# Optimization experiments

Measured on AMD Instinct MI355X. Metric: run time of the kernel, lower is better.

Reference implementation:

```python
import jax, jax.numpy as jnp
import numpy as np

BATCH, T, N_STATE, N_IN, N_OUT = 256, 4096, 32, 8, 8
DT = 1e-3


def setup_inputs() -> dict:
    key = jax.random.key(0)
    k_u, k_x0, k_A, k_B, k_C, k_D = jax.random.split(key, 6)
    t = jnp.arange(T, dtype=jnp.float32) * DT
    u = jax.random.normal(k_u, (BATCH, T, N_IN), dtype=jnp.float32)
    x0 = jax.random.normal(k_x0, (BATCH, N_STATE), dtype=jnp.float32)
    # Stable-ish LTI system parameters
    A = (0.1 / np.sqrt(N_STATE)) * jax.random.normal(k_A, (N_STATE, N_STATE), dtype=jnp.float32) - 0.5 * jnp.eye(N_STATE, dtype=jnp.float32)
    B = jax.random.normal(k_B, (N_STATE, N_IN), dtype=jnp.float32) / np.sqrt(N_IN)
    C = jax.random.normal(k_C, (N_OUT, N_STATE), dtype=jnp.float32) / np.sqrt(N_STATE)
    D = jax.random.normal(k_D, (N_OUT, N_IN), dtype=jnp.float32) / np.sqrt(N_IN)
    return {"t": t, "u": u, "x0": x0, "A": A, "B": B, "C": C, "D": D}


def _dopri5_solve(t, u, x0, A, B):
    """Fixed-step Dopri5 (Dormand-Prince 5th order) on a uniform grid.

    Mirrors diffrax.diffeqsolve(Dopri5, ConstantStepSize, dt0=t[1], saveat=ts=t):
    one RK step per grid interval. u is evaluated at stage times via linear
    interpolation between grid samples.
    """
    dt = t[1] - t[0]

    def f(x, uu):  # vector field: dx = A x + B u
        return x @ A.T + uu @ B.T

    ut = jnp.swapaxes(u, 0, 1)  # [T, BATCH, N_IN]

    def step(x, uu):
        u0, u1 = uu
        du = u1 - u0
        k1 = f(x, u0)
        k2 = f(x + dt * (0.2 * k1), u0 + 0.2 * du)
        k3 = f(x + dt * (3.0 / 40.0 * k1 + 9.0 / 40.0 * k2), u0 + 0.3 * du)
        k4 = f(x + dt * (44.0 / 45.0 * k1 - 56.0 / 15.0 * k2 + 32.0 / 9.0 * k3), u0 + 0.8 * du)
        k5 = f(x + dt * (19372.0 / 6561.0 * k1 - 25360.0 / 2187.0 * k2 + 64448.0 / 6561.0 * k3 - 212.0 / 729.0 * k4), u0 + (8.0 / 9.0) * du)
        k6 = f(x + dt * (9017.0 / 3168.0 * k1 - 355.0 / 33.0 * k2 + 46732.0 / 5247.0 * k3 + 49.0 / 176.0 * k4 - 5103.0 / 18656.0 * k5), u1)
        xn = x + dt * (35.0 / 384.0 * k1 + 500.0 / 1113.0 * k3 + 125.0 / 192.0 * k4 - 2187.0 / 6784.0 * k5 + 11.0 / 84.0 * k6)
        return xn, xn

    _, xs_rest = jax.lax.scan(step, x0, (ut[:-1], ut[1:]))
    xs = jnp.concatenate([x0[None], xs_rest], axis=0)  # [T, BATCH, N_STATE]
    return jnp.swapaxes(xs, 0, 1)  # [BATCH, T, N_STATE]


def reference(t, u, x0, A, B, C, D):
    xs = _dopri5_solve(t, u, x0, A, B)          # state trajectory [BATCH, T, N_STATE]
    ys = xs @ C.T + u @ D.T                      # output y = C x + D u, [BATCH, T, N_OUT]
    return xs, ys
```

## Files before the change

kernel.cpp:

```cpp
#include <hip/hip_runtime.h>

#define BATCH 256
#define TT 4096
#define NS 32
#define NI 8
#define NO 8
#define LCH 64
#define NCHUNKS 64

#define WS_M  0
#define WS_N0 1024
#define WS_N1 1280
#define WS_ML 1536
#define WS_V  2560
#define WS_S  (2560 + BATCH * NCHUNKS * NS)
#define WS_F  (WS_S + BATCH * NCHUNKS * NS)

__device__ __forceinline__ float dot4(float4 a, float4 b) {
    return a.x * b.x + a.y * b.y + a.z * b.z + a.w * b.w;
}
__device__ __forceinline__ float4 ld4(const float* p) { return *(const float4*)p; }

__global__ __launch_bounds__(256) void k_pre(const float* __restrict__ tarr,
                                             const float* __restrict__ A,
                                             const float* __restrict__ B,
                                             float* __restrict__ ws) {
    __shared__ float sA[NS * NS], sB[NS * NI];
    __shared__ float Ka[6][NS * NS];
    __shared__ float Kb[6][NS * NI];
    __shared__ float Kc[6][NS * NI];
    __shared__ float Sa[NS * NS], Sb[NS * NI], Sc[NS * NI];
    __shared__ float Pq[2][NS * NS];
    __shared__ float Ms[NS * NS];
    __shared__ float Ff[2][NS * NI];

    const int tid = threadIdx.x;
    const float dt = tarr[1] - tarr[0];

    for (int e = tid; e < NS * NS; e += 256) sA[e] = A[e];
    for (int e = tid; e < NS * NI; e += 256) sB[e] = B[e];
    __syncthreads();
    for (int e = tid; e < NS * NS; e += 256) Ka[0][e] = sA[e];
    for (int e = tid; e < NS * NI; e += 256) { Kb[0][e] = sB[e]; Kc[0][e] = 0.f; }
    __syncthreads();

    const float atab[5][5] = {
        {0.2f, 0.f, 0.f, 0.f, 0.f},
        {3.f / 40.f, 9.f / 40.f, 0.f, 0.f, 0.f},
        {44.f / 45.f, -56.f / 15.f, 32.f / 9.f, 0.f, 0.f},
        {19372.f / 6561.f, -25360.f / 2187.f, 64448.f / 6561.f, -212.f / 729.f, 0.f},
        {9017.f / 3168.f, -355.f / 33.f, 46732.f / 5247.f, 49.f / 176.f, -5103.f / 18656.f}};
    const float ctab[6] = {0.f, 0.2f, 0.3f, 0.8f, 8.f / 9.f, 1.f};

    for (int st = 1; st <= 5; ++st) {
        for (int e = tid; e < NS * NS; e += 256) {
            float acc = 0.f;
            for (int j = 0; j < st; ++j) acc += atab[st - 1][j] * Ka[j][e];
            Sa[e] = acc;
        }
        for (int e = tid; e < NS * NI; e += 256) {
            float ab = 0.f, ac = 0.f;
            for (int j = 0; j < st; ++j) {
                ab += atab[st - 1][j] * Kb[j][e];
                ac += atab[st - 1][j] * Kc[j][e];
            }
            Sb[e] = ab; Sc[e] = ac;
        }
        __syncthreads();
        {
            const int j = tid & 31, ig = tid >> 5;
            for (int r = 0; r < 4; ++r) {
                const int row = ig + 8 * r;
                float acc = 0.f;
                for (int k = 0; k < NS; ++k) acc += sA[row * NS + k] * Sa[k * NS + j];
                Ka[st][row * NS + j] = sA[row * NS + j] + dt * acc;
            }
            const int jb = tid & 7, rb = tid >> 3;
            float ab = 0.f, ac = 0.f;
            for (int k = 0; k < NS; ++k) {
                ab += sA[rb * NS + k] * Sb[k * NI + jb];
                ac += sA[rb * NS + k] * Sc[k * NI + jb];
            }
            Kb[st][rb * NI + jb] = sB[rb * NI + jb] + dt * ab;
            Kc[st][rb * NI + jb] = ctab[st] * sB[rb * NI + jb] + dt * ac;
        }
        __syncthreads();
    }

    const float btab[6] = {35.f / 384.f, 0.f, 500.f / 1113.f, 125.f / 192.f,
                           -2187.f / 6784.f, 11.f / 84.f};
    for (int e = tid; e < NS * NS; e += 256) {
        float acc = 0.f;
        for (int i2 = 0; i2 < 6; ++i2) acc += btab[i2] * Ka[i2][e];
        const float m = dt * acc + (((e / NS) == (e % NS)) ? 1.f : 0.f);
        ws[WS_M + e] = m;
        Pq[0][e] = m;
        Ms[e] = m;
    }
    for (int e = tid; e < NS * NI; e += 256) {
        float ap = 0.f, aq = 0.f;
        for (int i2 = 0; i2 < 6; ++i2) {
            ap += btab[i2] * Kb[i2][e];
            aq += btab[i2] * Kc[i2][e];
        }
        const float P = dt * ap, Q = dt * aq;
        ws[WS_N0 + e] = P - Q;
        ws[WS_N1 + e] = Q;
        Sb[e] = P - Q;
        Sc[e] = Q;
    }
    __syncthreads();

    int cur = 0;
    for (int itq = 0; itq < 6; ++itq) {
        const int j = tid & 31, ig = tid >> 5;
        for (int r = 0; r < 4; ++r) {
            const int row = ig + 8 * r;
            float acc = 0.f;
            for (int k = 0; k < NS; ++k) acc += Pq[cur][row * NS + k] * Pq[cur][k * NS + j];
            Pq[cur ^ 1][row * NS + j] = acc;
        }
        __syncthreads();
        cur ^= 1;
    }
    for (int e = tid; e < NS * NS; e += 256) ws[WS_ML + e] = Pq[cur][e];

    Ff[0][tid] = Sc[tid];
    ws[WS_F + 64 * NS * NI + tid] = Sc[tid];
    __syncthreads();
    int fc = 0;
    const int rr = tid >> 3, mm = tid & 7;
    for (int j = 63; j >= 0; --j) {
        float acc = 0.f;
#pragma unroll
        for (int k = 0; k < NS; ++k) acc += Ms[rr * NS + k] * Ff[fc][k * NI + mm];
        if (j == 63) acc += Sb[tid];
        Ff[fc ^ 1][tid] = acc;
        ws[WS_F + j * NS * NI + tid] = acc;
        __syncthreads();
        fc ^= 1;
    }
}

__global__ __launch_bounds__(256, 2) void k_phase1(const float* __restrict__ u,
                                                   float* __restrict__ ws) {
    __shared__ float4 sF[64 * 64];

    const int tid = threadIdx.x;

    const float4* Fg = (const float4*)(ws + WS_F);
    for (int idx = tid; idx < 64 * 64; idx += 256) {
        const int j = idx >> 6, r = idx & 63;
        sF[(j << 6) + ((r & 7) << 3) + (r >> 3)] = Fg[idx];
    }
    __syncthreads();

    const int task = blockIdx.x * 4 + (tid >> 6);
    const int c = task % (NCHUNKS - 1), g = task / (NCHUNKS - 1);
    const int l = tid & 63;
    const int beta = l >> 3, s8 = l & 7;
    const int b = g * 8 + beta;
    const int t0 = c * LCH;
    const float* ub = u + ((size_t)b * TT + t0) * NI;

    float4 ua = ld4(ub), uc = ld4(ub + 4);
    float a0 = 0.f, a1 = 0.f, a2 = 0.f, a3 = 0.f;

#pragma unroll 4
    for (int j = 0; j < 64; ++j) {
        const float4 na = ld4(ub + (j + 1) * NI);
        const float4 nb = ld4(ub + (j + 1) * NI + 4);
        const float4* fj = &sF[(j << 6) + s8];
        const float4 f0 = fj[0], f1 = fj[8], f2 = fj[16], f3 = fj[24];
        const float4 f4 = fj[32], f5 = fj[40], f6 = fj[48], f7 = fj[56];
        a0 += dot4(f0, ua) + dot4(f1, uc);
        a1 += dot4(f2, ua) + dot4(f3, uc);
        a2 += dot4(f4, ua) + dot4(f5, uc);
        a3 += dot4(f6, ua) + dot4(f7, uc);
        ua = na; uc = nb;
    }

    const float* Ft = ws + WS_F + 64 * (NS * NI) + 32 * s8;
    a0 += dot4(ld4(Ft), ua) + dot4(ld4(Ft + 4), uc);
    a1 += dot4(ld4(Ft + 8), ua) + dot4(ld4(Ft + 12), uc);
    a2 += dot4(ld4(Ft + 16), ua) + dot4(ld4(Ft + 20), uc);
    a3 += dot4(ld4(Ft + 24), ua) + dot4(ld4(Ft + 28), uc);

    *(float4*)(ws + WS_V + ((size_t)b * NCHUNKS + c) * NS + 4 * s8) =
        make_float4(a0, a1, a2, a3);
}

__global__ __launch_bounds__(64) void k_phase2(const float* __restrict__ x0,
                                               float* __restrict__ ws) {
    const float* ML = ws + WS_ML;
    const float* v = ws + WS_V;
    float* sst = ws + WS_S;
    const int b = blockIdx.x;
    const int l = threadIdx.x, i = l & 31, h = l >> 5;

    float mlr[16];
#pragma unroll
    for (int jj = 0; jj < 16; ++jj) mlr[jj] = ML[i * NS + 16 * h + jj];

    float x = x0[b * NS + i];
    for (int c = 0; c < NCHUNKS; ++c) {
        if (h == 0) sst[((size_t)b * NCHUNKS + c) * NS + i] = x;
        if (c == NCHUNKS - 1) break;
        float p = 0.f;
#pragma unroll
        for (int jj = 0; jj < 16; ++jj) p += mlr[jj] * __shfl(x, 16 * h + jj, 64);
        p += __shfl_xor(p, 32, 64);
        x = p + v[((size_t)b * NCHUNKS + c) * NS + i];
    }
}

__global__ __launch_bounds__(64, 1) void k_phase3(const float* __restrict__ u,
                                                  float* __restrict__ ws,
                                                  float* __restrict__ out,
                                                  const float* __restrict__ Cc,
                                                  const float* __restrict__ Dd) {
    const float* M = ws + WS_M;
    const float* N0 = ws + WS_N0;
    const float* N1 = ws + WS_N1;

    const int task = blockIdx.x;
    const int c = task % NCHUNKS, g = task / NCHUNKS;
    const int l = threadIdx.x;
    const int beta = l >> 3, s8 = l & 7;
    const int b = g * 8 + beta;

    float4 mq[4][8];
#pragma unroll
    for (int r = 0; r < 4; ++r)
#pragma unroll
        for (int jj = 0; jj < 8; ++jj) mq[r][jj] = ld4(M + (4 * s8 + r) * NS + 4 * jj);

    float4 n0q[4][2], n1q[4][2];
#pragma unroll
    for (int r = 0; r < 4; ++r) {
        n0q[r][0] = ld4(N0 + (4 * s8 + r) * NI);
        n0q[r][1] = ld4(N0 + (4 * s8 + r) * NI + 4);
        n1q[r][0] = ld4(N1 + (4 * s8 + r) * NI);
        n1q[r][1] = ld4(N1 + (4 * s8 + r) * NI + 4);
    }

    float4 cq[8], dq[2];
#pragma unroll
    for (int jj = 0; jj < 8; ++jj) cq[jj] = ld4(Cc + s8 * NS + 4 * jj);
    dq[0] = ld4(Dd + s8 * NI);
    dq[1] = ld4(Dd + s8 * NI + 4);

    __shared__ float4 xb[2][8 * 9];

    const int t0 = c * LCH;
    const float* ub = u + (size_t)b * TT * NI;
    float4 u0a = ld4(ub + t0 * NI), u0b = ld4(ub + t0 * NI + 4);
    float4 u1a = ld4(ub + (t0 + 1) * NI), u1b = ld4(ub + (t0 + 1) * NI + 4);

    float4 mine = ld4(ws + WS_S + ((size_t)b * NCHUNKS + c) * NS + 4 * s8);
    xb[0][beta * 9 + s8] = mine;
    asm volatile("s_waitcnt lgkmcnt(0)" ::: "memory");
    __builtin_amdgcn_sched_barrier(0);

    float* yout = out + (size_t)BATCH * TT * NS;
    int cur = 0;
    for (int js = 0; js < LCH; ++js) {
        const int t = t0 + js;
        float4 xq[8];
#pragma unroll
        for (int jj = 0; jj < 8; ++jj) xq[jj] = xb[cur][beta * 9 + jj];

        const int tp = (t + 2 < TT - 1) ? (t + 2) : (TT - 1);
        const float4 u2a = ld4(ub + tp * NI);
        const float4 u2b = ld4(ub + tp * NI + 4);

        *(float4*)(out + ((size_t)b * TT + t) * NS + 4 * s8) = mine;
        float yv = 0.f;
#pragma unroll
        for (int jj = 0; jj < 8; ++jj) yv += dot4(cq[jj], xq[jj]);
        yv += dot4(dq[0], u0a) + dot4(dq[1], u0b);
        yout[((size_t)b * TT + t) * NO + s8] = yv;

        if (js < LCH - 1) {
            float w0 = dot4(n0q[0][0], u0a) + dot4(n0q[0][1], u0b) + dot4(n1q[0][0], u1a) + dot4(n1q[0][1], u1b);
            float w1 = dot4(n0q[1][0], u0a) + dot4(n0q[1][1], u0b) + dot4(n1q[1][0], u1a) + dot4(n1q[1][1], u1b);
            float w2 = dot4(n0q[2][0], u0a) + dot4(n0q[2][1], u0b) + dot4(n1q[2][0], u1a) + dot4(n1q[2][1], u1b);
            float w3 = dot4(n0q[3][0], u0a) + dot4(n0q[3][1], u0b) + dot4(n1q[3][0], u1a) + dot4(n1q[3][1], u1b);
#pragma unroll
            for (int jj = 0; jj < 8; ++jj) {
                const float4 xv = xq[jj];
                w0 += dot4(mq[0][jj], xv);
                w1 += dot4(mq[1][jj], xv);
                w2 += dot4(mq[2][jj], xv);
                w3 += dot4(mq[3][jj], xv);
            }
            mine = make_float4(w0, w1, w2, w3);
            xb[cur ^ 1][beta * 9 + s8] = mine;
            u0a = u1a; u0b = u1b;
            u1a = u2a; u1b = u2b;
        }
        asm volatile("s_waitcnt lgkmcnt(0)" ::: "memory");
        __builtin_amdgcn_sched_barrier(0);
        cur ^= 1;
    }
}

extern "C" void kernel_launch(void* const* d_in, const int* in_sizes, int n_in,
                              void* d_out, int out_size, void* d_ws, size_t ws_size,
                              hipStream_t stream) {
    const float* t = (const float*)d_in[0];
    const float* u = (const float*)d_in[1];
    const float* x0 = (const float*)d_in[2];
    const float* A = (const float*)d_in[3];
    const float* B = (const float*)d_in[4];
    const float* C = (const float*)d_in[5];
    const float* D = (const float*)d_in[6];
    float* out = (float*)d_out;
    float* ws = (float*)d_ws;

    k_pre<<<dim3(1), dim3(256), 0, stream>>>(t, A, B, ws);
    k_phase1<<<dim3(8 * (NCHUNKS - 1)), dim3(256), 0, stream>>>(u, ws);
    k_phase2<<<dim3(BATCH), dim3(64), 0, stream>>>(x0, ws);
    k_phase3<<<dim3(32 * NCHUNKS), dim3(64), 0, stream>>>(u, ws, out, C, D);
}
```

Baseline: 353.3 us.

## Parallelize forcing-term chain, transpose sF load, raise phase3 occupancy, shorten u prefetch

In k_pre, the 64-step serial recurrence building the chunk forcing matrices is split into two levels. A M^8 power is captured from the repeated-squaring loop, 8 stride-8 seeds are built, and each is then advanced with M seven times, with matrix rows held in registers and fewer barriers. k_phase1 now reads the F table from global memory in transposed order so its shared-memory writes are contiguous. k_phase3 raises launch bounds to 3 waves per SIMD and loads the next u sample at the start of each step rather than two steps ahead. That trades prefetch depth for fewer live registers.

Result: slower. 1.333 ms (+277.2%).

```diff
diff --git a/kernel.cpp b/kernel.cpp
--- a/kernel.cpp
+++ b/kernel.cpp
@@ -32,7 +32,6 @@
     __shared__ float Sa[NS * NS], Sb[NS * NI], Sc[NS * NI];
     __shared__ float Pq[2][NS * NS];
     __shared__ float Ms[NS * NS];
-    __shared__ float Ff[2][NS * NI];
 
     const int tid = threadIdx.x;
     const float dt = tarr[1] - tarr[0];
@@ -122,24 +121,54 @@
         }
         __syncthreads();
         cur ^= 1;
+        if (itq == 2)
+            for (int e = tid; e < NS * NS; e += 256) Sa[e] = Pq[cur][e];
     }
     for (int e = tid; e < NS * NS; e += 256) ws[WS_ML + e] = Pq[cur][e];
 
-    Ff[0][tid] = Sc[tid];
-    ws[WS_F + 64 * NS * NI + tid] = Sc[tid];
-    __syncthreads();
-    int fc = 0;
+    float* cb = &Ka[0][0];
     const int rr = tid >> 3, mm = tid & 7;
-    for (int j = 63; j >= 0; --j) {
+
+    float mrow[NS], m8row[NS];
+#pragma unroll
+    for (int kk = 0; kk < NS; ++kk) { mrow[kk] = Ms[rr * NS + kk]; m8row[kk] = Sa[rr * NS + kk]; }
+
+    {
         float acc = 0.f;
 #pragma unroll
-        for (int k = 0; k < NS; ++k) acc += Ms[rr * NS + k] * Ff[fc][k * NI + mm];
-        if (j == 63) acc += Sb[tid];
-        Ff[fc ^ 1][tid] = acc;
-        ws[WS_F + j * NS * NI + tid] = acc;
-        __syncthreads();
-        fc ^= 1;
-    }
+        for (int kk = 0; kk < NS; ++kk) acc += mrow[kk] * Sc[kk * NI + mm];
+        const float h = Sb[tid] + acc;
+        cb[tid] = h;
+        ws[WS_F + 63 * (NS * NI) + tid] = h;
+    }
+    __syncthreads();
+    for (int i = 1; i < 8; ++i) {
+        float acc = 0.f;
+#pragma unroll
+        for (int kk = 0; kk < NS; ++kk) acc += m8row[kk] * cb[(i - 1) * 256 + kk * NI + mm];
+        cb[i * 256 + tid] = acc;
+        ws[WS_F + (63 - 8 * i) * (NS * NI) + tid] = acc;
+        __syncthreads();
+    }
+    int pp = 0;
+    for (int k = 1; k < 8; ++k) {
+        float acc[8];
+#pragma unroll
+        for (int i = 0; i < 8; ++i) {
+            float a = 0.f;
+#pragma unroll
+            for (int kk = 0; kk < NS; ++kk) a += mrow[kk] * cb[pp * 2048 + i * 256 + kk * NI + mm];
+            acc[i] = a;
+        }
+#pragma unroll
+        for (int i = 0; i < 8; ++i) {
+            cb[(pp ^ 1) * 2048 + i * 256 + tid] = acc[i];
+            ws[WS_F + (63 - 8 * i - k) * (NS * NI) + tid] = acc[i];
+        }
+        __syncthreads();
+        pp ^= 1;
+    }
+    ws[WS_F + 64 * (NS * NI) + tid] = Sc[tid];
 }
 
 __global__ __launch_bounds__(256, 2) void k_phase1(const float* __restrict__ u,
@@ -150,8 +179,8 @@
 
     const float4* Fg = (const float4*)(ws + WS_F);
     for (int idx = tid; idx < 64 * 64; idx += 256) {
-        const int j = idx >> 6, r = idx & 63;
-        sF[(j << 6) + ((r & 7) << 3) + (r >> 3)] = Fg[idx];
+        const int j = idx >> 6, q = (idx >> 3) & 7, s = idx & 7;
+        sF[idx] = Fg[(j << 6) + (s << 3) + q];
     }
     __syncthreads();
 
@@ -214,7 +243,7 @@
     }
 }
 
-__global__ __launch_bounds__(64, 1) void k_phase3(const float* __restrict__ u,
+__global__ __launch_bounds__(64, 3) void k_phase3(const float* __restrict__ u,
                                                   float* __restrict__ ws,
                                                   float* __restrict__ out,
                                                   const float* __restrict__ Cc,
@@ -255,7 +284,6 @@
     const int t0 = c * LCH;
     const float* ub = u + (size_t)b * TT * NI;
     float4 u0a = ld4(ub + t0 * NI), u0b = ld4(ub + t0 * NI + 4);
-    float4 u1a = ld4(ub + (t0 + 1) * NI), u1b = ld4(ub + (t0 + 1) * NI + 4);
 
     float4 mine = ld4(ws + WS_S + ((size_t)b * NCHUNKS + c) * NS + 4 * s8);
     xb[0][beta * 9 + s8] = mine;
@@ -270,10 +298,6 @@
 #pragma unroll
         for (int jj = 0; jj < 8; ++jj) xq[jj] = xb[cur][beta * 9 + jj];
 
-        const int tp = (t + 2 < TT - 1) ? (t + 2) : (TT - 1);
-        const float4 u2a = ld4(ub + tp * NI);
-        const float4 u2b = ld4(ub + tp * NI + 4);
-
         *(float4*)(out + ((size_t)b * TT + t) * NS + 4 * s8) = mine;
         float yv = 0.f;
 #pragma unroll
@@ -282,10 +306,12 @@
         yout[((size_t)b * TT + t) * NO + s8] = yv;
 
         if (js < LCH - 1) {
-            float w0 = dot4(n0q[0][0], u0a) + dot4(n0q[0][1], u0b) + dot4(n1q[0][0], u1a) + dot4(n1q[0][1], u1b);
-            float w1 = dot4(n0q[1][0], u0a) + dot4(n0q[1][1], u0b) + dot4(n1q[1][0], u1a) + dot4(n1q[1][1], u1b);
-            float w2 = dot4(n0q[2][0], u0a) + dot4(n0q[2][1], u0b) + dot4(n1q[2][0], u1a) + dot4(n1q[2][1], u1b);
-            float w3 = dot4(n0q[3][0], u0a) + dot4(n0q[3][1], u0b) + dot4(n1q[3][0], u1a) + dot4(n1q[3][1], u1b);
+            const float4 u1a = ld4(ub + (t + 1) * NI);
+            const float4 u1b = ld4(ub + (t + 1) * NI + 4);
+            float w0 = dot4(n0q[0][0], u0a) + dot4(n0q[0][1], u0b);
+            float w1 = dot4(n0q[1][0], u0a) + dot4(n0q[1][1], u0b);
+            float w2 = dot4(n0q[2][0], u0a) + dot4(n0q[2][1], u0b);
+            float w3 = dot4(n0q[3][0], u0a) + dot4(n0q[3][1], u0b);
 #pragma unroll
             for (int jj = 0; jj < 8; ++jj) {
                 const float4 xv = xq[jj];
@@ -294,10 +320,13 @@
                 w2 += dot4(mq[2][jj], xv);
                 w3 += dot4(mq[3][jj], xv);
             }
+            w0 += dot4(n1q[0][0], u1a) + dot4(n1q[0][1], u1b);
+            w1 += dot4(n1q[1][0], u1a) + dot4(n1q[1][1], u1b);
+            w2 += dot4(n1q[2][0], u1a) + dot4(n1q[2][1], u1b);
+            w3 += dot4(n1q[3][0], u1a) + dot4(n1q[3][1], u1b);
             mine = make_float4(w0, w1, w2, w3);
             xb[cur ^ 1][beta * 9 + s8] = mine;
             u0a = u1a; u0b = u1b;
-            u1a = u2a; u1b = u2b;
         }
         asm volatile("s_waitcnt lgkmcnt(0)" ::: "memory");
         __builtin_amdgcn_sched_barrier(0);
```
